# Performance work log

Measured on AMD Instinct MI355X. Metric: run time of the kernel, lower is better.

Reference implementation:

```python
import jax, jax.numpy as jnp
import numpy as np

E = 1024      # emb_dim
H = 16        # num_heads
DH = E // H   # per-head atten_dim
B = 2
T = 2048


def _layernorm(x, scale, shift, eps=1e-5):
    mean = x.mean(axis=-1, keepdims=True)
    var = ((x - mean) ** 2).mean(axis=-1, keepdims=True)  # unbiased=False
    return scale * (x - mean) / jnp.sqrt(var + eps) + shift


def _gelu(x):
    # Faithful to source: tanh(sqrt(2/pi)*x + 0.044715*x^3)  (no sqrt on cubic term)
    c = jnp.sqrt(jnp.asarray(2.0 / jnp.pi, x.dtype))
    return 0.5 * x * (1.0 + jnp.tanh(c * x + 0.044715 * x ** 3))


def setup_inputs() -> dict:
    key = jax.random.key(0)
    ks = jax.random.split(key, 12)
    s = 0.02
    return {
        "x":     jax.random.normal(ks[0], (B, T, E), jnp.float32),
        "Wq":    jax.random.normal(ks[1], (H, E, DH), jnp.float32) * s,
        "Wk":    jax.random.normal(ks[2], (H, E, DH), jnp.float32) * s,
        "Wv":    jax.random.normal(ks[3], (H, E, DH), jnp.float32) * s,
        "fc_w":  jax.random.normal(ks[4], (E, E), jnp.float32) * s,
        "fc_b":  jnp.zeros((E,), jnp.float32),
        "ln1_s": jnp.ones((E,), jnp.float32),
        "ln1_b": jnp.zeros((E,), jnp.float32),
        "ln2_s": jnp.ones((E,), jnp.float32),
        "ln2_b": jnp.zeros((E,), jnp.float32),
        "ff_w1": jax.random.normal(ks[5], (E, 4 * E), jnp.float32) * s,
        "ff_b1": jnp.zeros((4 * E,), jnp.float32),
        "ff_w2": jax.random.normal(ks[6], (4 * E, E), jnp.float32) * s,
        "ff_b2": jnp.zeros((E,), jnp.float32),
    }


def _attention(x, Wq, Wk, Wv, fc_w, fc_b):
    b, t, _ = x.shape
    q = jnp.einsum("bte,hed->bhtd", x, Wq)
    k = jnp.einsum("bte,hed->bhtd", x, Wk)
    v = jnp.einsum("bte,hed->bhtd", x, Wv)
    scores = jnp.einsum("bhtd,bhsd->bhts", q, k)
    causal = jnp.triu(jnp.ones((t, t), bool), 1)
    scores = jnp.where(causal, -jnp.inf, scores)
    w = jax.nn.softmax(scores / jnp.sqrt(jnp.asarray(DH, x.dtype)), axis=-1)
    ctx = jnp.einsum("bhts,bhsd->bhtd", w, v)
    # faithful quirk from source: per-head transpose(1,2) then reshape(b, T, d_out)
    ctx = jnp.swapaxes(ctx, 2, 3).reshape(b, H, t, DH)
    concat = ctx.transpose(0, 2, 1, 3).reshape(b, t, E)
    return concat @ fc_w + fc_b


def reference(x, Wq, Wk, Wv, fc_w, fc_b, ln1_s, ln1_b, ln2_s, ln2_b,
              ff_w1, ff_b1, ff_w2, ff_b2):
    h = _attention(_layernorm(x, ln1_s, ln1_b), Wq, Wk, Wv, fc_w, fc_b) + x
    y = _layernorm(h, ln2_s, ln2_b)
    y = _gelu(y @ ff_w1 + ff_b1) @ ff_w2 + ff_b2
    return y + h
```

## Files before the change

kernel.cpp:

```cpp
#include <hip/hip_runtime.h>


#define En 1024
#define Hn 16
#define DHn 64
#define Bn 2
#define Tn 2048
#define Mrows 4096

typedef __attribute__((ext_vector_type(8))) short bf16x8;
typedef __attribute__((ext_vector_type(4))) float f32x4;

__device__ __forceinline__ short f2bf(float f) {
    unsigned u = __float_as_uint(f);
    u += 0x7FFFu + ((u >> 16) & 1u);
    return (short)(u >> 16);
}
__device__ __forceinline__ ushort f2bfu(float f) {
    unsigned u = __float_as_uint(f);
    u += 0x7FFFu + ((u >> 16) & 1u);
    return (ushort)(u >> 16);
}
__device__ __forceinline__ float bf2f(ushort u) {
    return __uint_as_float((unsigned)u << 16);
}

__device__ __forceinline__ float gelu_f(float x) {
    float u = 0.79788456080286535588f * x + 0.044715f * x * x * x;
    float t = __expf(2.0f * u);
    return x * t / (t + 1.0f);
}

__device__ __forceinline__ void load_lds16(const void* g, void* l) {
    __builtin_amdgcn_global_load_lds(
        (const __attribute__((address_space(1))) unsigned int*)(uintptr_t)g,
        (__attribute__((address_space(3))) unsigned int*)(uintptr_t)l,
        16, 0, 0);
}

__global__ __launch_bounds__(256) void ln_kernel(
    const float* __restrict__ in, const float* __restrict__ sc,
    const float* __restrict__ sh, ushort* __restrict__ out)
{
    int row = blockIdx.x;
    int tid = threadIdx.x;
    float4 v = ((const float4*)(in + (size_t)row * En))[tid];
    float s  = v.x + v.y + v.z + v.w;
    float s2 = v.x*v.x + v.y*v.y + v.z*v.z + v.w*v.w;
    #pragma unroll
    for (int off = 32; off > 0; off >>= 1) {
        s  += __shfl_down(s,  off);
        s2 += __shfl_down(s2, off);
    }
    __shared__ float red[2][4];
    int wave = tid >> 6, lane = tid & 63;
    if (lane == 0) { red[0][wave] = s; red[1][wave] = s2; }
    __syncthreads();
    s  = red[0][0] + red[0][1] + red[0][2] + red[0][3];
    s2 = red[1][0] + red[1][1] + red[1][2] + red[1][3];
    float mean = s * (1.0f / En);
    float var  = s2 * (1.0f / En) - mean * mean;
    float r = rsqrtf(var + 1e-5f);
    float4 scv = ((const float4*)sc)[tid];
    float4 shv = ((const float4*)sh)[tid];
    ushort4 o;
    o.x = f2bfu(scv.x * (v.x - mean) * r + shv.x);
    o.y = f2bfu(scv.y * (v.y - mean) * r + shv.y);
    o.z = f2bfu(scv.z * (v.z - mean) * r + shv.z);
    o.w = f2bfu(scv.w * (v.w - mean) * r + shv.w);
    ((ushort4*)(out + (size_t)row * En))[tid] = o;
}

__global__ __launch_bounds__(256) void ln2_fuse(
    const ushort* __restrict__ P0, const ushort* __restrict__ P1,
    const float* __restrict__ bias, const float* __restrict__ x,
    const float* __restrict__ sc, const float* __restrict__ sh,
    ushort* __restrict__ hb, ushort* __restrict__ ynb)
{
    int row = blockIdx.x, tid = threadIdx.x;
    size_t idx = (size_t)row * 256 + tid;
    ushort4 a = ((const ushort4*)P0)[idx];
    ushort4 b = ((const ushort4*)P1)[idx];
    float4 bi = ((const float4*)bias)[tid];
    float4 xr = ((const float4*)x)[idx];
    float4 v;
    v.x = bf2f(a.x) + bf2f(b.x) + bi.x + xr.x;
    v.y = bf2f(a.y) + bf2f(b.y) + bi.y + xr.y;
    v.z = bf2f(a.z) + bf2f(b.z) + bi.z + xr.z;
    v.w = bf2f(a.w) + bf2f(b.w) + bi.w + xr.w;
    ushort4 hv;
    hv.x = f2bfu(v.x); hv.y = f2bfu(v.y); hv.z = f2bfu(v.z); hv.w = f2bfu(v.w);
    ((ushort4*)hb)[idx] = hv;
    float s  = v.x + v.y + v.z + v.w;
    float s2 = v.x*v.x + v.y*v.y + v.z*v.z + v.w*v.w;
    #pragma unroll
    for (int off = 32; off > 0; off >>= 1) {
        s  += __shfl_down(s,  off);
        s2 += __shfl_down(s2, off);
    }
    __shared__ float red[2][4];
    int wave = tid >> 6, lane = tid & 63;
    if (lane == 0) { red[0][wave] = s; red[1][wave] = s2; }
    __syncthreads();
    s  = red[0][0] + red[0][1] + red[0][2] + red[0][3];
    s2 = red[1][0] + red[1][1] + red[1][2] + red[1][3];
    float mean = s * (1.0f / En);
    float var  = s2 * (1.0f / En) - mean * mean;
    float r = rsqrtf(var + 1e-5f);
    float4 scv = ((const float4*)sc)[tid];
    float4 shv = ((const float4*)sh)[tid];
    ushort4 o;
    o.x = f2bfu(scv.x * (v.x - mean) * r + shv.x);
    o.y = f2bfu(scv.y * (v.y - mean) * r + shv.y);
    o.z = f2bfu(scv.z * (v.z - mean) * r + shv.z);
    o.w = f2bfu(scv.w * (v.w - mean) * r + shv.w);
    ((ushort4*)ynb)[idx] = o;
}

__global__ __launch_bounds__(256) void ff2_reduce4(
    const ushort* __restrict__ P, const float* __restrict__ bias,
    const ushort* __restrict__ hb, float* __restrict__ out)
{
    int tid = threadIdx.x;
    size_t i = (size_t)blockIdx.x * 256 + tid;
    const size_t S = (size_t)Mrows * En / 4;
    ushort4 a = ((const ushort4*)P)[i];
    ushort4 b = ((const ushort4*)P)[i + S];
    ushort4 c = ((const ushort4*)P)[i + 2 * S];
    ushort4 d = ((const ushort4*)P)[i + 3 * S];
    float4 bi = ((const float4*)bias)[tid];
    ushort4 hu = ((const ushort4*)hb)[i];
    float4 o;
    o.x = (bf2f(a.x) + bf2f(b.x)) + (bf2f(c.x) + bf2f(d.x)) + bi.x + bf2f(hu.x);
    o.y = (bf2f(a.y) + bf2f(b.y)) + (bf2f(c.y) + bf2f(d.y)) + bi.y + bf2f(hu.y);
    o.z = (bf2f(a.z) + bf2f(b.z)) + (bf2f(c.z) + bf2f(d.z)) + bi.z + bf2f(hu.z);
    o.w = (bf2f(a.w) + bf2f(b.w)) + (bf2f(c.w) + bf2f(d.w)) + bi.w + bf2f(hu.w);
    ((float4*)out)[i] = o;
}

__global__ __launch_bounds__(256) void prep_w(
    const float* __restrict__ Wq, const float* __restrict__ Wk,
    const float* __restrict__ Wv, const float* __restrict__ fc_w,
    const float* __restrict__ ff_w1, const float* __restrict__ ff_w2,
    ushort* __restrict__ wqkv, ushort* __restrict__ wfc,
    ushort* __restrict__ wf1, ushort* __restrict__ wf2)
{
    int bid = blockIdx.x;
    const float* in; ushort* out; int N, ldo, k0, n0;
    if (bid < 768) {
        int z = bid >> 4, kb = bid & 15;
        int sel = z / 16, h = z % 16;
        in  = (sel == 0 ? Wq : sel == 1 ? Wk : Wv) + (size_t)h * En * DHn;
        out = wqkv + (size_t)(sel * 1024 + h * 64) * En;
        N = DHn; ldo = En; k0 = kb * 64; n0 = 0;
    } else if (bid < 1024) {
        int b2 = bid - 768;
        in = fc_w; out = wfc; N = En; ldo = En;
        k0 = (b2 & 15) * 64; n0 = (b2 >> 4) * 64;
    } else if (bid < 2048) {
        int b2 = bid - 1024;
        in = ff_w1; out = wf1; N = 4 * En; ldo = En;
        k0 = (b2 & 15) * 64; n0 = (b2 >> 4) * 64;
    } else {
        int b2 = bid - 2048;
        in = ff_w2; out = wf2; N = En; ldo = 4 * En;
        k0 = (b2 & 63) * 64; n0 = (b2 >> 6) * 64;
    }
    __shared__ float t[64][65];
    int tid = threadIdx.x, r = tid >> 4, c4 = (tid & 15) * 4;
    #pragma unroll
    for (int i = 0; i < 4; ++i) {
        float4 v = *(const float4*)(in + (size_t)(k0 + r + i * 16) * N + n0 + c4);
        t[r + i * 16][c4 + 0] = v.x; t[r + i * 16][c4 + 1] = v.y;
        t[r + i * 16][c4 + 2] = v.z; t[r + i * 16][c4 + 3] = v.w;
    }
    __syncthreads();
    #pragma unroll
    for (int i = 0; i < 4; ++i) {
        int n = r + i * 16;
        ushort4 u;
        u.x = f2bfu(t[c4 + 0][n]); u.y = f2bfu(t[c4 + 1][n]);
        u.z = f2bfu(t[c4 + 2][n]); u.w = f2bfu(t[c4 + 3][n]);
        *(ushort4*)(out + (size_t)(n0 + n) * ldo + k0 + c4) = u;
    }
}

template<int MODE, int TN>
__global__ __launch_bounds__(256) void gemm_bf16(
    const ushort* __restrict__ A, int lda,
    const ushort* __restrict__ Bt, int ldb, int Kloop,
    const float* __restrict__ bias,
    ushort* __restrict__ Cb, int ldc,
    ushort* __restrict__ qo, ushort* __restrict__ ko, ushort* __restrict__ vo)
{
    constexpr int WCN = TN / 2;
    constexpr int NI  = WCN / 16;
    constexpr int BIW = TN * 8 / 256;
    constexpr int STAGE = 128 * 64 + TN * 64;
    constexpr int BOUNCE = (MODE == 2 || MODE == 1) ? 4 * 64 * 68
                         : (MODE == 3 ? 128 * 68 : 0);
    constexpr int SMEMN = STAGE > BOUNCE ? STAGE : BOUNCE;
    __shared__ ushort smem[SMEMN];
    ushort* As = smem;
    ushort* Bs = smem + 128 * 64;
    int tid = threadIdx.x, wv = tid >> 6, lid = tid & 63;
    int m0 = blockIdx.x * 128, n0 = blockIdx.y * TN;
    int koff = blockIdx.z * Kloop;
    int wr = wv >> 1, wc = wv & 1;
    int hm = lid & 15, hk = lid >> 4;

    f32x4 acc[4][NI];
    #pragma unroll
    for (int i = 0; i < 4; ++i)
        #pragma unroll
        for (int j = 0; j < NI; ++j) acc[i][j] = (f32x4){0.f, 0.f, 0.f, 0.f};

    const ushort* Abase = A + (size_t)m0 * lda + koff;
    const ushort* Bbase = Bt + (size_t)n0 * ldb + koff;

    for (int k0 = 0; k0 < Kloop; k0 += 64) {
        __syncthreads();
        #pragma unroll
        for (int i = 0; i < 4; ++i) {
            int c = wv * 256 + i * 64 + lid;
            int r = c >> 3, s = c & 7;
            int j = s ^ (r & 7);
            load_lds16(Abase + (size_t)r * lda + k0 + j * 8,
                       &As[(wv * 256 + i * 64) * 8]);
        }
        #pragma unroll
        for (int i = 0; i < BIW; ++i) {
            int c = wv * (BIW * 64) + i * 64 + lid;
            int r = c >> 3, s = c & 7;
            int j = s ^ (r & 7);
            load_lds16(Bbase + (size_t)r * ldb + k0 + j * 8,
                       &Bs[(wv * (BIW * 64) + i * 64) * 8]);
        }
        __syncthreads();
        #pragma unroll
        for (int kk = 0; kk < 2; ++kk) {
            bf16x8 af[4], bfr[NI];
            #pragma unroll
            for (int mi = 0; mi < 4; ++mi) {
                int r = wr * 64 + mi * 16 + hm;
                int slot = ((kk << 2) | hk) ^ (r & 7);
                af[mi] = *(const bf16x8*)&As[(r * 8 + slot) * 8];
            }
            #pragma unroll
            for (int ni = 0; ni < NI; ++ni) {
                int r = wc * WCN + ni * 16 + hm;
                int slot = ((kk << 2) | hk) ^ (r & 7);
                bfr[ni] = *(const bf16x8*)&Bs[(r * 8 + slot) * 8];
            }
            #pragma unroll
            for (int mi = 0; mi < 4; ++mi)
                #pragma unroll
                for (int ni = 0; ni < NI; ++ni)
                    acc[mi][ni] = __builtin_amdgcn_mfma_f32_16x16x32_bf16(
                        af[mi], bfr[ni], acc[mi][ni], 0, 0, 0);
        }
    }

    int colbase = n0 + wc * WCN + hm;
    int rowbase = m0 + wr * 64 + hk * 4;
    if (MODE == 1) {
        __syncthreads();
        ushort* Ls = smem + wv * (64 * 68);
        #pragma unroll
        for (int ni = 0; ni < NI; ++ni) {
            int col = colbase + ni * 16;
            float bb = bias[col];
            #pragma unroll
            for (int mi = 0; mi < 4; ++mi)
                #pragma unroll
                for (int r = 0; r < 4; ++r)
                    Ls[(mi * 16 + hk * 4 + r) * 68 + ni * 16 + hm] =
                        f2bfu(gelu_f(acc[mi][ni][r] + bb));
        }
        ushort* outp = Cb + (size_t)(m0 + wr * 64) * ldc + n0 + wc * 64;
        int dcol = hm * 4;
        #pragma unroll
        for (int i = 0; i < 16; ++i) {
            int t = hk + i * 4;
            *(ushort4*)(outp + (size_t)t * ldc + dcol) =
                *(const ushort4*)&Ls[t * 68 + dcol];
        }
    } else if (MODE == 2) {
        __syncthreads();
        ushort* Ls = smem + wv * (64 * 68);
        int col0 = n0 + wc * 64;
        int sel = col0 >> 10, h = (col0 & 1023) >> 6;
        if (sel < 2) {
            #pragma unroll
            for (int ni = 0; ni < NI; ++ni)
                #pragma unroll
                for (int mi = 0; mi < 4; ++mi)
                    #pragma unroll
                    for (int r = 0; r < 4; ++r)
                        Ls[(mi * 16 + hk * 4 + r) * 68 + ni * 16 + hm] =
                            f2bfu(acc[mi][ni][r]);
            ushort* outp = (sel == 0 ? qo : ko) + (size_t)h * (Mrows * DHn);
            int dcol = hm * 4;
            #pragma unroll
            for (int i = 0; i < 16; ++i) {
                int t = hk + i * 4;
                *(ushort4*)(outp + (size_t)(m0 + wr * 64 + t) * DHn + dcol) =
                    *(const ushort4*)&Ls[t * 68 + dcol];
            }
        } else {
            #pragma unroll
            for (int ni = 0; ni < NI; ++ni)
                #pragma unroll
                for (int mi = 0; mi < 4; ++mi)
                    #pragma unroll
                    for (int r = 0; r < 4; ++r)
                        Ls[(ni * 16 + hm) * 68 + mi * 16 + hk * 4 + r] =
                            f2bfu(acc[mi][ni][r]);
            int bb2 = m0 >> 11;
            int t0 = (m0 & 2047) + wr * 64;
            ushort* outp = vo + ((size_t)((h * 2 + bb2) * 64)) * Tn + t0;
            int tcol = hm * 4;
            #pragma unroll
            for (int i = 0; i < 16; ++i) {
                int d = hk + i * 4;
                *(ushort4*)(outp + (size_t)d * Tn + tcol) =
                    *(const ushort4*)&Ls[d * 68 + tcol];
            }
        }
    } else {
        __syncthreads();
        ushort* Ls = smem;
        #pragma unroll
        for (int ni = 0; ni < NI; ++ni)
            #pragma unroll
            for (int mi = 0; mi < 4; ++mi)
                #pragma unroll
                for (int r = 0; r < 4; ++r)
                    Ls[(wr * 64 + mi * 16 + hk * 4 + r) * 68
                       + wc * WCN + ni * 16 + hm] = f2bfu(acc[mi][ni][r]);
        __syncthreads();
        ushort* Cp = Cb + (size_t)blockIdx.z * Mrows * ldc;
        #pragma unroll
        for (int it = 0; it < 8; ++it) {
            int i = it * 1024 + tid * 4;
            int row = i >> 6, col = i & 63;
            *(ushort4*)(Cp + (size_t)(m0 + row) * ldc + n0 + col) =
                *(const ushort4*)&Ls[row * 68 + col];
        }
    }
}

#define PHASE_MID() do { \
    __builtin_amdgcn_s_barrier(); \
    asm volatile("s_waitcnt lgkmcnt(0)" ::: "memory"); \
    __builtin_amdgcn_sched_barrier(0); \
} while (0)

#define LOAD_AF(MH, KK) \
    _Pragma("unroll") \
    for (int mi = 0; mi < 4; ++mi) { \
        int r = wr * 128 + (MH) * 64 + mi * 16 + hm; \
        af[mi] = *(const bf16x8*)&As_[(r * 8 + ((((KK) << 2) | hk) ^ (r & 7))) * 8]; \
    }

#define MFMA_PHASE(MH, KK) do { \
    __builtin_amdgcn_s_setprio(1); \
    _Pragma("unroll") \
    for (int mi = 0; mi < 4; ++mi) \
        _Pragma("unroll") \
        for (int ni = 0; ni < 4; ++ni) \
            acc[(MH) * 4 + mi][ni] = __builtin_amdgcn_mfma_f32_16x16x32_bf16( \
                af[mi], bfr[KK][ni], acc[(MH) * 4 + mi][ni], 0, 0, 0); \
    __builtin_amdgcn_s_setprio(0); \
} while (0)

#define STAGE_A(bufp, h, ksrc) do { \
    ushort* _d = smem + (bufp) * 32768; \
    load_lds16(Abase + aoff[h][0] + (ksrc), _d + ldsoff[h][0]); \
    load_lds16(Abase + aoff[h][1] + (ksrc), _d + ldsoff[h][1]); \
} while (0)

#define STAGE_B(bufp, h, ksrc) do { \
    ushort* _d = smem + (bufp) * 32768 + 16384; \
    load_lds16(Bbase + boff[h][0] + (ksrc), _d + ldsoff[h][0]); \
    load_lds16(Bbase + boff[h][1] + (ksrc), _d + ldsoff[h][1]); \
} while (0)

template<int MODE>
__global__ __launch_bounds__(512, 2) void gemm256(
    const ushort* __restrict__ A, int lda,
    const ushort* __restrict__ Bt, int ldb, int Kloop,
    const float* __restrict__ bias,
    ushort* __restrict__ Cb, int ldc,
    ushort* __restrict__ qo, ushort* __restrict__ ko, ushort* __restrict__ vo)
{
    __shared__ ushort smem[65536];
    int tid = threadIdx.x, wv = tid >> 6, lid = tid & 63;
    int wr = wv >> 2, wc = wv & 3;
    int hm = lid & 15, hk = lid >> 4;
    int m0 = blockIdx.x * 256, n0 = blockIdx.y * 256;
    int koff = blockIdx.z * Kloop;
    int NT = Kloop >> 6;

    const ushort* Abase = A + (size_t)m0 * lda + koff;
    const ushort* Bbase = Bt + (size_t)n0 * ldb + koff;

    int aoff[2][2], boff[2][2], ldsoff[2][2];
    #pragma unroll
    for (int h = 0; h < 2; ++h)
        #pragma unroll
        for (int i = 0; i < 2; ++i) {
            int c = h * 1024 + wv * 128 + i * 64 + lid;
            int r = c >> 3, s = c & 7, j = s ^ (r & 7);
            aoff[h][i] = r * lda + j * 8;
            boff[h][i] = r * ldb + j * 8;
            ldsoff[h][i] = (h * 1024 + wv * 128 + i * 64) * 8;
        }

    f32x4 acc[8][4];
    #pragma unroll
    for (int i = 0; i < 8; ++i)
        #pragma unroll
        for (int j = 0; j < 4; ++j) acc[i][j] = (f32x4){0.f, 0.f, 0.f, 0.f};

    STAGE_A(0, 0, 0); STAGE_A(0, 1, 0);
    STAGE_B(0, 0, 0); STAGE_B(0, 1, 0);
    {
        int k1 = (NT > 1 ? 1 : 0) << 6;
        STAGE_B(1, 0, k1); STAGE_B(1, 1, k1);
    }
    asm volatile("s_waitcnt vmcnt(4)" ::: "memory");
    __builtin_amdgcn_s_barrier();

    for (int t = 0; t < NT; ++t) {
        int cur = t & 1, nxt = cur ^ 1;
        int kA = (t + 1 < NT ? t + 1 : NT - 1) << 6;
        int kB = (t + 2 < NT ? t + 2 : NT - 1) << 6;
        const ushort* As_ = smem + cur * 32768;
        const ushort* Bs_ = As_ + 16384;
        bf16x8 af[4], bfr[2][4];

        LOAD_AF(0, 0);
        #pragma unroll
        for (int kk = 0; kk < 2; ++kk)
            #pragma unroll
            for (int ni = 0; ni < 4; ++ni) {
                int r = wc * 64 + ni * 16 + hm;
                bfr[kk][ni] = *(const bf16x8*)
                    &Bs_[(r * 8 + (((kk << 2) | hk) ^ (r & 7))) * 8];
            }
        STAGE_A(nxt, 0, kA);
        PHASE_MID();
        MFMA_PHASE(0, 0);
        __builtin_amdgcn_s_barrier();

        LOAD_AF(1, 0);
        STAGE_A(nxt, 1, kA);
        PHASE_MID();
        MFMA_PHASE(1, 0);
        __builtin_amdgcn_s_barrier();

        LOAD_AF(0, 1);
        STAGE_B(cur, 0, kB);
        PHASE_MID();
        MFMA_PHASE(0, 1);
        __builtin_amdgcn_s_barrier();

        LOAD_AF(1, 1);
        STAGE_B(cur, 1, kB);
        PHASE_MID();
        MFMA_PHASE(1, 1);
        asm volatile("s_waitcnt vmcnt(4)" ::: "memory");
        __builtin_amdgcn_s_barrier();
    }
    asm volatile("s_waitcnt vmcnt(0)" ::: "memory");
    __builtin_amdgcn_s_barrier();

    ushort* Ls = smem + wv * (64 * 68);
    int dcol = hm * 4;
    if (MODE == 1) {
        float bb[4];
        #pragma unroll
        for (int ni = 0; ni < 4; ++ni) bb[ni] = bias[n0 + wc * 64 + ni * 16 + hm];
        #pragma unroll
        for (int mh = 0; mh < 2; ++mh) {
            #pragma unroll
            for (int ni = 0; ni < 4; ++ni)
                #pragma unroll
                for (int mi = 0; mi < 4; ++mi)
                    #pragma unroll
                    for (int r = 0; r < 4; ++r)
                        Ls[(mi * 16 + hk * 4 + r) * 68 + ni * 16 + hm] =
                            f2bfu(gelu_f(acc[mh * 4 + mi][ni][r] + bb[ni]));
            ushort* outp = Cb + (size_t)(m0 + wr * 128 + mh * 64) * ldc
                              + n0 + wc * 64;
            #pragma unroll
            for (int i = 0; i < 16; ++i) {
                int tt = hk + i * 4;
                *(ushort4*)(outp + (size_t)tt * ldc + dcol) =
                    *(const ushort4*)&Ls[tt * 68 + dcol];
            }
        }
    } else if (MODE == 2) {
        int col0 = n0 + wc * 64;
        int sel = col0 >> 10, hh = (col0 & 1023) >> 6;
        #pragma unroll
        for (int mh = 0; mh < 2; ++mh) {
            int rowb = m0 + wr * 128 + mh * 64;
            if (sel < 2) {
                #pragma unroll
                for (int ni = 0; ni < 4; ++ni)
                    #pragma unroll
                    for (int mi = 0; mi < 4; ++mi)
                        #pragma unroll
                        for (int r = 0; r < 4; ++r)
                            Ls[(mi * 16 + hk * 4 + r) * 68 + ni * 16 + hm] =
                                f2bfu(acc[mh * 4 + mi][ni][r]);
                ushort* outp = (sel == 0 ? qo : ko) + (size_t)hh * (Mrows * DHn);
                #pragma unroll
                for (int i = 0; i < 16; ++i) {
                    int tt = hk + i * 4;
                    *(ushort4*)(outp + (size_t)(rowb + tt) * DHn + dcol) =
                        *(const ushort4*)&Ls[tt * 68 + dcol];
                }
            } else {
                #pragma unroll
                for (int ni = 0; ni < 4; ++ni)
                    #pragma unroll
                    for (int mi = 0; mi < 4; ++mi)
                        #pragma unroll
                        for (int r = 0; r < 4; ++r)
                            Ls[(ni * 16 + hm) * 68 + mi * 16 + hk * 4 + r] =
                                f2bfu(acc[mh * 4 + mi][ni][r]);
                int bb2 = m0 >> 11;
                int t0 = (m0 & 2047) + wr * 128 + mh * 64;
                ushort* outp = vo + ((size_t)((hh * 2 + bb2) * 64)) * Tn + t0;
                #pragma unroll
                for (int i = 0; i < 16; ++i) {
                    int d = hk + i * 4;
                    *(ushort4*)(outp + (size_t)d * Tn + dcol) =
                        *(const ushort4*)&Ls[d * 68 + dcol];
                }
            }
        }
    } else {
        ushort* Cp = Cb + (size_t)blockIdx.z * ((size_t)Mrows * ldc);
        #pragma unroll
        for (int mh = 0; mh < 2; ++mh) {
            #pragma unroll
            for (int ni = 0; ni < 4; ++ni)
                #pragma unroll
                for (int mi = 0; mi < 4; ++mi)
                    #pragma unroll
                    for (int r = 0; r < 4; ++r)
                        Ls[(mi * 16 + hk * 4 + r) * 68 + ni * 16 + hm] =
                            f2bfu(acc[mh * 4 + mi][ni][r]);
            ushort* outp = Cp + (size_t)(m0 + wr * 128 + mh * 64) * ldc
                              + n0 + wc * 64;
            #pragma unroll
            for (int i = 0; i < 16; ++i) {
                int tt = hk + i * 4;
                *(ushort4*)(outp + (size_t)tt * ldc + dcol) =
                    *(const ushort4*)&Ls[tt * 68 + dcol];
            }
        }
    }
}

__global__ __launch_bounds__(512) void attn_mfma(
    const ushort* __restrict__ q, const ushort* __restrict__ ksrc,
    const ushort* __restrict__ vtsrc, ushort* __restrict__ cat)
{
    int g = blockIdx.x;
    int h = g >> 1, b = g & 1;
    const ushort* qg  = q     + (size_t)g * Tn * DHn;
    const ushort* kg  = ksrc  + (size_t)g * Tn * DHn;
    const ushort* vtg = vtsrc + (size_t)g * DHn * Tn;
    int tid = threadIdx.x, w = tid >> 6, lane = tid & 63;
    int m = lane & 15, gq = lane >> 4;

    __shared__ short Ks[2][4096];
    __shared__ short Vt[2][4096];
    __shared__ short Ps[8][1024];

    int R = tid >> 3;
    int c = tid & 7;
    int slot = R * 64 + ((c ^ (R & 7)) << 3);
    const ushort* kbase = kg  + (size_t)R * DHn + c * 8;
    const ushort* vbase = vtg + (size_t)R * Tn  + c * 8;

    #pragma unroll 1
    for (int phase = 0; phase < 2; ++phase) {
        int qj = phase ? (15 - (int)blockIdx.y) : (int)blockIdx.y;
        int q0 = qj * 128;
        int NT = 2 * qj + 2;
        int qb = q0 + w * 16;

        bf16x8 qf[2];
        {
            const ushort* qp = qg + (size_t)(qb + m) * DHn + gq * 8;
            qf[0] = *(const bf16x8*)(qp);
            qf[1] = *(const bf16x8*)(qp + 32);
        }
        f32x4 o[4];
        #pragma unroll
        for (int i = 0; i < 4; ++i) o[i] = (f32x4){0.f, 0.f, 0.f, 0.f};
        float lsum[4] = {0.f, 0.f, 0.f, 0.f};

        bf16x8 kreg = *(const bf16x8*)(kbase);
        bf16x8 vreg = *(const bf16x8*)(vbase);
        *(bf16x8*)&Ks[0][slot] = kreg;
        *(bf16x8*)&Vt[0][slot] = vreg;
        __syncthreads();

        #pragma unroll 1
        for (int kt = 0; kt < NT; ++kt) {
            int cur = kt & 1;
            if (kt + 1 < NT) {
                kreg = *(const bf16x8*)(kbase + (size_t)(kt + 1) * 4096);
                vreg = *(const bf16x8*)(vbase + (kt + 1) * 64);
            }
            if (qb >= kt * 64) {
                float ps[4][4];
                #pragma unroll
                for (int ct = 0; ct < 4; ++ct) {
                    int dk = kt * 64 + ct * 16 - qb;
                    if (dk > 0) {
                        ps[ct][0] = ps[ct][1] = ps[ct][2] = ps[ct][3] = 0.f;
                        continue;
                    }
                    f32x4 acc = (f32x4){0.f, 0.f, 0.f, 0.f};
                    int row = ct * 16 + m;
                    __builtin_amdgcn_s_setprio(1);
                    #pragma unroll
                    for (int db = 0; db < 2; ++db) {
                        bf16x8 kf = *(const bf16x8*)
                            &Ks[cur][row * 64 + (((db * 4 + gq) ^ (row & 7)) << 3)];
                        acc = __builtin_amdgcn_mfma_f32_16x16x32_bf16(
                            qf[db], kf, acc, 0, 0, 0);
                    }
                    __builtin_amdgcn_s_setprio(0);
                    #pragma unroll
                    for (int r = 0; r < 4; ++r) {
                        float p;
                        if (dk == 0 && m > gq * 4 + r) p = 0.f;
                        else p = __expf(acc[r] * 0.125f);
                        ps[ct][r] = p;
                        lsum[r] += p;
                    }
                }

                #pragma unroll
                for (int ct = 0; ct < 4; ++ct)
                    #pragma unroll
                    for (int r = 0; r < 4; ++r) {
                        int prow = gq * 4 + r;
                        Ps[w][prow * 64 +
                              ((((ct * 2 + (m >> 3)) ^ (prow & 7)) << 3) | (m & 7))] =
                            f2bf(ps[ct][r]);
                    }
                bf16x8 pf[2];
                #pragma unroll
                for (int db2 = 0; db2 < 2; ++db2)
                    pf[db2] = *(const bf16x8*)
                        &Ps[w][m * 64 + (((db2 * 4 + gq) ^ (m & 7)) << 3)];

                __builtin_amdgcn_s_setprio(1);
                #pragma unroll
                for (int ct2 = 0; ct2 < 4; ++ct2) {
                    int row = ct2 * 16 + m;
                    #pragma unroll
                    for (int db2 = 0; db2 < 2; ++db2) {
                        bf16x8 vf = *(const bf16x8*)
                            &Vt[cur][row * 64 + (((db2 * 4 + gq) ^ (row & 7)) << 3)];
                        o[ct2] = __builtin_amdgcn_mfma_f32_16x16x32_bf16(
                            pf[db2], vf, o[ct2], 0, 0, 0);
                    }
                }
                __builtin_amdgcn_s_setprio(0);
            }
            if (kt + 1 < NT) {
                int nb = (kt + 1) & 1;
                *(bf16x8*)&Ks[nb][slot] = kreg;
                *(bf16x8*)&Vt[nb][slot] = vreg;
            }
            __syncthreads();
        }

        float inv[4];
        #pragma unroll
        for (int r = 0; r < 4; ++r) {
            float l = lsum[r];
            l += __shfl_xor(l, 1);
            l += __shfl_xor(l, 2);
            l += __shfl_xor(l, 4);
            l += __shfl_xor(l, 8);
            inv[r] = 1.0f / l;
        }
        int qt_old = (q0 >> 6) + (w >> 2);
        int wv_old = w & 3;
        size_t base = (size_t)b * Tn * En + (size_t)h * 64 + (size_t)qt_old * En
                    + wv_old * 16 + gq * 4;
        #pragma unroll
        for (int ct2 = 0; ct2 < 4; ++ct2) {
            int d = ct2 * 16 + m;
            #pragma unroll
            for (int r = 0; r < 4; ++r)
                cat[base + (size_t)d * 32 * En + r] = f2bfu(o[ct2][r] * inv[r]);
        }
    }
}

extern "C" void kernel_launch(void* const* d_in, const int* in_sizes, int n_in,
                              void* d_out, int out_size, void* d_ws, size_t ws_size,
                              hipStream_t stream) {
    const float* x     = (const float*)d_in[0];
    const float* Wq    = (const float*)d_in[1];
    const float* Wk    = (const float*)d_in[2];
    const float* Wv    = (const float*)d_in[3];
    const float* fc_w  = (const float*)d_in[4];
    const float* fc_b  = (const float*)d_in[5];
    const float* ln1_s = (const float*)d_in[6];
    const float* ln1_b = (const float*)d_in[7];
    const float* ln2_s = (const float*)d_in[8];
    const float* ln2_b = (const float*)d_in[9];
    const float* ff_w1 = (const float*)d_in[10];
    const float* ff_b1 = (const float*)d_in[11];
    const float* ff_w2 = (const float*)d_in[12];
    const float* ff_b2 = (const float*)d_in[13];
    float* out = (float*)d_out;
    (void)in_sizes; (void)n_in; (void)out_size; (void)ws_size;

    const size_t MB = 1048576;
    char* w8 = (char*)d_ws;
    ushort* S0   = (ushort*)(w8 + 0 * MB);
    ushort* kb   = (ushort*)(w8 + 8 * MB);
    ushort* vtb  = (ushort*)(w8 + 16 * MB);
    ushort* qb   = (ushort*)(w8 + 24 * MB);
    ushort* hb   = (ushort*)(w8 + 32 * MB);
    ushort* Pfc  = (ushort*)(w8 + 48 * MB);
    ushort* y1   = (ushort*)(w8 + 48 * MB);
    ushort* Pff2 = (ushort*)(w8 + 0 * MB);
    ushort* wqkv = (ushort*)(w8 + 80 * MB);
    ushort* wfc  = (ushort*)(w8 + 86 * MB);
    ushort* wf1  = (ushort*)(w8 + 88 * MB);
    ushort* wf2  = (ushort*)(w8 + 96 * MB);

    prep_w<<<dim3(3072), 256, 0, stream>>>(
        Wq, Wk, Wv, fc_w, ff_w1, ff_w2, wqkv, wfc, wf1, wf2);

    ln_kernel<<<dim3(Mrows), 256, 0, stream>>>(x, ln1_s, ln1_b, S0);
    gemm256<2><<<dim3(16, 12), 512, 0, stream>>>(
        S0, En, wqkv, En, En, nullptr, nullptr, 0, qb, kb, vtb);
    attn_mfma<<<dim3(Hn * Bn, 8), 512, 0, stream>>>(qb, kb, vtb, S0);
    gemm_bf16<3, 64><<<dim3(32, 16, 2), 256, 0, stream>>>(
        S0, En, wfc, En, En / 2, nullptr, Pfc, En, nullptr, nullptr, nullptr);
    ln2_fuse<<<dim3(Mrows), 256, 0, stream>>>(
        Pfc, Pfc + (size_t)Mrows * En, fc_b, x, ln2_s, ln2_b, hb, qb);
    gemm256<1><<<dim3(16, 16), 512, 0, stream>>>(
        qb, En, wf1, En, En, ff_b1, y1, 4 * En, nullptr, nullptr, nullptr);
    gemm256<3><<<dim3(16, 4, 4), 512, 0, stream>>>(
        y1, 4 * En, wf2, 4 * En, En, nullptr, Pff2, En, nullptr, nullptr, nullptr);
    ff2_reduce4<<<dim3(Mrows), 256, 0, stream>>>(Pff2, ff_b2, hb, out);
}
```

Measured before the change: 324.2 us.

## Process two key tiles per barrier and transpose QK MFMA for packed P stores

The attention kernel now stages two 64-key tiles per double-buffer round, which halves the number of __syncthreads and prefetch rounds. The QK^T MFMA operands are swapped so each lane holds a row of scores in one query column. Probabilities are then packed with v_cvt_pk_bf16 and written to LDS as 8-byte stores instead of scalar 2-byte scatters, and the row-sum reduction is reworked to match. The cost is doubled K/V LDS usage, which may reduce occupancy.

```diff
diff --git a/kernel.cpp b/kernel.cpp
--- a/kernel.cpp
+++ b/kernel.cpp
@@ -23,6 +23,11 @@
 }
 __device__ __forceinline__ float bf2f(ushort u) {
     return __uint_as_float((unsigned)u << 16);
+}
+__device__ __forceinline__ unsigned cvt_pk_bf16(float lo, float hi) {
+    unsigned r;
+    asm("v_cvt_pk_bf16_f32 %0, %1, %2" : "=v"(r) : "v"(lo), "v"(hi));
+    return r;
 }
 
 __device__ __forceinline__ float gelu_f(float x) {
@@ -262,7 +267,6 @@
     }
 
     int colbase = n0 + wc * WCN + hm;
-    int rowbase = m0 + wr * 64 + hk * 4;
     if (MODE == 1) {
         __syncthreads();
         ushort* Ls = smem + wv * (64 * 68);
@@ -578,9 +582,10 @@
     const ushort* vtg = vtsrc + (size_t)g * DHn * Tn;
     int tid = threadIdx.x, w = tid >> 6, lane = tid & 63;
     int m = lane & 15, gq = lane >> 4;
-
-    __shared__ short Ks[2][4096];
-    __shared__ short Vt[2][4096];
+    int qoff = gq * 4;
+
+    __shared__ short Ks[2][2][4096];
+    __shared__ short Vt[2][2][4096];
     __shared__ short Ps[8][1024];
 
     int R = tid >> 3;
@@ -593,7 +598,7 @@
     for (int phase = 0; phase < 2; ++phase) {
         int qj = phase ? (15 - (int)blockIdx.y) : (int)blockIdx.y;
         int q0 = qj * 128;
-        int NT = 2 * qj + 2;
+        int NR = qj + 1;
         int qb = q0 + w * 16;
 
         bf16x8 qf[2];
@@ -605,98 +610,113 @@
         f32x4 o[4];
         #pragma unroll
         for (int i = 0; i < 4; ++i) o[i] = (f32x4){0.f, 0.f, 0.f, 0.f};
-        float lsum[4] = {0.f, 0.f, 0.f, 0.f};
-
-        bf16x8 kreg = *(const bf16x8*)(kbase);
-        bf16x8 vreg = *(const bf16x8*)(vbase);
-        *(bf16x8*)&Ks[0][slot] = kreg;
-        *(bf16x8*)&Vt[0][slot] = vreg;
+        float lsum = 0.f;
+
+        {
+            bf16x8 a0 = *(const bf16x8*)(kbase);
+            bf16x8 a1 = *(const bf16x8*)(kbase + 4096);
+            bf16x8 b0 = *(const bf16x8*)(vbase);
+            bf16x8 b1 = *(const bf16x8*)(vbase + 64);
+            *(bf16x8*)&Ks[0][0][slot] = a0;
+            *(bf16x8*)&Ks[0][1][slot] = a1;
+            *(bf16x8*)&Vt[0][0][slot] = b0;
+            *(bf16x8*)&Vt[0][1][slot] = b1;
+        }
         __syncthreads();
 
         #pragma unroll 1
-        for (int kt = 0; kt < NT; ++kt) {
-            int cur = kt & 1;
-            if (kt + 1 < NT) {
-                kreg = *(const bf16x8*)(kbase + (size_t)(kt + 1) * 4096);
-                vreg = *(const bf16x8*)(vbase + (kt + 1) * 64);
-            }
-            if (qb >= kt * 64) {
-                float ps[4][4];
+        for (int rd = 0; rd < NR; ++rd) {
+            int cur = rd & 1;
+            bf16x8 k0r, k1r, v0r, v1r;
+            bool pre = (rd + 1 < NR);
+            if (pre) {
+                k0r = *(const bf16x8*)(kbase + (size_t)(2 * rd + 2) * 4096);
+                k1r = *(const bf16x8*)(kbase + (size_t)(2 * rd + 3) * 4096);
+                v0r = *(const bf16x8*)(vbase + (2 * rd + 2) * 64);
+                v1r = *(const bf16x8*)(vbase + (2 * rd + 3) * 64);
+            }
+            #pragma unroll
+            for (int hf = 0; hf < 2; ++hf) {
+                int kt = 2 * rd + hf;
+                const short* Kt_ = &Ks[cur][hf][0];
+                const short* Vt_ = &Vt[cur][hf][0];
+                if (qb < kt * 64) continue;
+
                 #pragma unroll
                 for (int ct = 0; ct < 4; ++ct) {
-                    int dk = kt * 64 + ct * 16 - qb;
-                    if (dk > 0) {
-                        ps[ct][0] = ps[ct][1] = ps[ct][2] = ps[ct][3] = 0.f;
-                        continue;
+                    int dk2 = kt * 64 + ct * 16 - qb;
+                    uint2 u;
+                    if (dk2 > 0) {
+                        u.x = 0u; u.y = 0u;
+                    } else {
+                        f32x4 acc = (f32x4){0.f, 0.f, 0.f, 0.f};
+                        int row = ct * 16 + m;
+                        __builtin_amdgcn_s_setprio(1);
+                        #pragma unroll
+                        for (int db = 0; db < 2; ++db) {
+                            bf16x8 kf = *(const bf16x8*)
+                                &Kt_[row * 64 + (((db * 4 + gq) ^ (row & 7)) << 3)];
+                            acc = __builtin_amdgcn_mfma_f32_16x16x32_bf16(
+                                kf, qf[db], acc, 0, 0, 0);
+                        }
+                        __builtin_amdgcn_s_setprio(0);
+                        float p0, p1, p2, p3;
+                        if (dk2 == 0) {
+                            p0 = (qoff + 0 > m) ? 0.f : __expf(acc[0] * 0.125f);
+                            p1 = (qoff + 1 > m) ? 0.f : __expf(acc[1] * 0.125f);
+                            p2 = (qoff + 2 > m) ? 0.f : __expf(acc[2] * 0.125f);
+                            p3 = (qoff + 3 > m) ? 0.f : __expf(acc[3] * 0.125f);
+                        } else {
+                            p0 = __expf(acc[0] * 0.125f);
+                            p1 = __expf(acc[1] * 0.125f);
+                            p2 = __expf(acc[2] * 0.125f);
+                            p3 = __expf(acc[3] * 0.125f);
+                        }
+                        lsum += (p0 + p1) + (p2 + p3);
+                        u.x = cvt_pk_bf16(p0, p1);
+                        u.y = cvt_pk_bf16(p2, p3);
                     }
-                    f32x4 acc = (f32x4){0.f, 0.f, 0.f, 0.f};
-                    int row = ct * 16 + m;
-                    __builtin_amdgcn_s_setprio(1);
-                    #pragma unroll
-                    for (int db = 0; db < 2; ++db) {
-                        bf16x8 kf = *(const bf16x8*)
-                            &Ks[cur][row * 64 + (((db * 4 + gq) ^ (row & 7)) << 3)];
-                        acc = __builtin_amdgcn_mfma_f32_16x16x32_bf16(
-                            qf[db], kf, acc, 0, 0, 0);
-                    }
-                    __builtin_amdgcn_s_setprio(0);
-                    #pragma unroll
-                    for (int r = 0; r < 4; ++r) {
-                        float p;
-                        if (dk == 0 && m > gq * 4 + r) p = 0.f;
-                        else p = __expf(acc[r] * 0.125f);
-                        ps[ct][r] = p;
-                        lsum[r] += p;
-                    }
+                    *(uint2*)&Ps[w][m * 64 +
+                        (((ct * 2 + (gq >> 1)) ^ (m & 7)) << 3) + ((gq & 1) << 2)] = u;
                 }
 
-                #pragma unroll
-                for (int ct = 0; ct < 4; ++ct)
-                    #pragma unroll
-                    for (int r = 0; r < 4; ++r) {
-                        int prow = gq * 4 + r;
-                        Ps[w][prow * 64 +
-                              ((((ct * 2 + (m >> 3)) ^ (prow & 7)) << 3) | (m & 7))] =
-                            f2bf(ps[ct][r]);
-                    }
-                bf16x8 pf[2];
-                #pragma unroll
-                for (int db2 = 0; db2 < 2; ++db2)
-                    pf[db2] = *(const bf16x8*)
-                        &Ps[w][m * 64 + (((db2 * 4 + gq) ^ (m & 7)) << 3)];
-
+                bf16x8 pf0 = *(const bf16x8*)
+                    &Ps[w][m * 64 + ((gq ^ (m & 7)) << 3)];
+                bf16x8 pf1 = *(const bf16x8*)
+                    &Ps[w][m * 64 + (((4 + gq) ^ (m & 7)) << 3)];
                 __builtin_amdgcn_s_setprio(1);
                 #pragma unroll
                 for (int ct2 = 0; ct2 < 4; ++ct2) {
                     int row = ct2 * 16 + m;
-                    #pragma unroll
-                    for (int db2 = 0; db2 < 2; ++db2) {
-                        bf16x8 vf = *(const bf16x8*)
-                            &Vt[cur][row * 64 + (((db2 * 4 + gq) ^ (row & 7)) << 3)];
-                        o[ct2] = __builtin_amdgcn_mfma_f32_16x16x32_bf16(
-                            pf[db2], vf, o[ct2], 0, 0, 0);
-                    }
+                    bf16x8 vf0 = *(const bf16x8*)
+                        &Vt_[row * 64 + ((gq ^ (row & 7)) << 3)];
+                    o[ct2] = __builtin_amdgcn_mfma_f32_16x16x32_bf16(
+                        pf0, vf0, o[ct2], 0, 0, 0);
+                    bf16x8 vf1 = *(const bf16x8*)
+                        &Vt_[row * 64 + (((4 + gq) ^ (row & 7)) << 3)];
+                    o[ct2] = __builtin_amdgcn_mfma_f32_16x16x32_bf16(
+                        pf1, vf1, o[ct2], 0, 0, 0);
                 }
                 __builtin_amdgcn_s_setprio(0);
             }
-            if (kt + 1 < NT) {
-                int nb = (kt + 1) & 1;
-                *(bf16x8*)&Ks[nb][slot] = kreg;
-                *(bf16x8*)&Vt[nb][slot] = vreg;
+            if (pre) {
+                int nb = cur ^ 1;
+                *(bf16x8*)&Ks[nb][0][slot] = k0r;
+                *(bf16x8*)&Ks[nb][1][slot] = k1r;
+                *(bf16x8*)&Vt[nb][0][slot] = v0r;
+                *(bf16x8*)&Vt[nb][1][slot] = v1r;
             }
             __syncthreads();
         }
 
+        float l = lsum;
+        l += __shfl_xor(l, 16);
+        l += __shfl_xor(l, 32);
         float inv[4];
         #pragma unroll
-        for (int r = 0; r < 4; ++r) {
-            float l = lsum[r];
-            l += __shfl_xor(l, 1);
-            l += __shfl_xor(l, 2);
-            l += __shfl_xor(l, 4);
-            l += __shfl_xor(l, 8);
-            inv[r] = 1.0f / l;
-        }
+        for (int r = 0; r < 4; ++r)
+            inv[r] = 1.0f / __shfl(l, qoff + r);
+
         int qt_old = (q0 >> 6) + (w >> 2);
         int wv_old = w & 3;
         size_t base = (size_t)b * Tn * En + (size_t)h * 64 + (size_t)qt_old * En
```

Measured after the change: 314.0 us. 3.2% less time.
